# Performance work log

Measured on AMD Instinct MI355X. Metric: run time of the kernel, lower is better.

The kernel has to match this reference:

```python
import jax, jax.numpy as jnp
import numpy as np

INPUT, HIDDEN, OUTPUT = 128, 256, 128
BATCH, SEQ = 64, 2048


def setup_inputs() -> dict:
    key = jax.random.key(0)
    ks = jax.random.split(key, 7)
    s_ih = 1.0 / np.sqrt(HIDDEN)
    x = jax.random.normal(ks[0], (BATCH, SEQ, INPUT), dtype=jnp.float32)
    W_ih = jax.random.uniform(ks[1], (HIDDEN, INPUT), jnp.float32, -s_ih, s_ih)
    W_hh = jax.random.uniform(ks[2], (HIDDEN, HIDDEN), jnp.float32, -s_ih, s_ih)
    b_ih = jax.random.uniform(ks[3], (HIDDEN,), jnp.float32, -s_ih, s_ih)
    b_hh = jax.random.uniform(ks[4], (HIDDEN,), jnp.float32, -s_ih, s_ih)
    s_fc = 1.0 / np.sqrt(HIDDEN)
    W_fc = jax.random.uniform(ks[5], (OUTPUT, HIDDEN), jnp.float32, -s_fc, s_fc)
    b_fc = jax.random.uniform(ks[6], (OUTPUT,), jnp.float32, -s_fc, s_fc)
    return {"x": x, "W_ih": W_ih, "W_hh": W_hh, "b_ih": b_ih,
            "b_hh": b_hh, "W_fc": W_fc, "b_fc": b_fc}


def reference(x, W_ih, W_hh, b_ih, b_hh, W_fc, b_fc):
    B = x.shape[0]
    # Precompute input projections for all timesteps: [S, B, H]
    xp = jnp.einsum('bsi,hi->sbh', x, W_ih) + b_ih + b_hh
    h0 = jnp.zeros((B, W_hh.shape[0]), dtype=x.dtype)

    def step(h, xp_t):
        h = jnp.tanh(xp_t + h @ W_hh.T)
        return h, None

    hT, _ = jax.lax.scan(step, h0, xp)
    return hT @ W_fc.T + b_fc
```

## Files before the change

### kernel.cpp

```cpp
#include <hip/hip_runtime.h>
#include <hip/hip_bf16.h>
#include <hip/hip_fp16.h>


#define S_LEN 2048
#define B_SZ  64
#define IN_D  128
#define HID   256
#define OUT_D 128

typedef _Float16 half2_t __attribute__((ext_vector_type(2)));
typedef _Float16 half8_t __attribute__((ext_vector_type(8)));
typedef float    f32x4   __attribute__((ext_vector_type(4)));

#if __has_builtin(__builtin_amdgcn_fdot2)
#define FDOT2(a, b, c) __builtin_amdgcn_fdot2((a), (b), (c), false)
#else
#define FDOT2(a, b, c) ((c) + (float)(a).x * (float)(b).x + (float)(a).y * (float)(b).y)
#endif

#if __has_builtin(__builtin_amdgcn_exp2f)
#define EXP2F(x) __builtin_amdgcn_exp2f(x)
#else
#define EXP2F(x) exp2f(x)
#endif

#if __has_builtin(__builtin_amdgcn_rcpf)
#define RCPF(x) __builtin_amdgcn_rcpf(x)
#else
#define RCPF(x) (1.0f / (x))
#endif

__global__ __launch_bounds__(256) void xproj_kernel(
    const float* __restrict__ x, const float* __restrict__ W_ih,
    const float* __restrict__ b_ih, const float* __restrict__ b_hh,
    _Float16* __restrict__ xp)
{
    const int lane  = threadIdx.x & 63;
    const int wave  = threadIdx.x >> 6;
    const int idx16 = lane & 15;
    const int kq    = lane >> 4;
    const int r0    = blockIdx.x * 256 + wave * 64;

    half8_t afr[4][4];
    #pragma unroll
    for (int mt = 0; mt < 4; ++mt) {
        #pragma unroll
        for (int sl = 0; sl < 4; ++sl) {
            const float4* ap = (const float4*)(x + (size_t)(r0 + mt * 16 + idx16) * IN_D + sl * 32 + kq * 8);
            float4 a0 = ap[0], a1 = ap[1];
            afr[mt][sl] = half8_t{(_Float16)a0.x, (_Float16)a0.y, (_Float16)a0.z, (_Float16)a0.w,
                                  (_Float16)a1.x, (_Float16)a1.y, (_Float16)a1.z, (_Float16)a1.w};
        }
    }

    for (int nc = 0; nc < 16; ++nc) {
        const int n0 = nc * 16;
        const float bias = b_ih[n0 + idx16] + b_hh[n0 + idx16];

        half8_t bfr[4];
        #pragma unroll
        for (int sl = 0; sl < 4; ++sl) {
            const float4* bp = (const float4*)(W_ih + (size_t)(n0 + idx16) * IN_D + sl * 32 + kq * 8);
            float4 b0 = bp[0], b1 = bp[1];
            bfr[sl] = half8_t{(_Float16)b0.x, (_Float16)b0.y, (_Float16)b0.z, (_Float16)b0.w,
                              (_Float16)b1.x, (_Float16)b1.y, (_Float16)b1.z, (_Float16)b1.w};
        }

        #pragma unroll
        for (int mt = 0; mt < 4; ++mt) {
            f32x4 acc = {0.f, 0.f, 0.f, 0.f};
            #pragma unroll
            for (int sl = 0; sl < 4; ++sl)
                acc = __builtin_amdgcn_mfma_f32_16x16x32_f16(afr[mt][sl], bfr[sl], acc, 0, 0, 0);
            #pragma unroll
            for (int r = 0; r < 4; ++r) {
                const int m = r0 + mt * 16 + kq * 4 + r;
                xp[(size_t)m * HID + n0 + idx16] = (_Float16)(acc[r] + bias);
            }
        }
    }
}

__global__ __launch_bounds__(1024) void rnn_kernel(
    const _Float16* __restrict__ xp, const float* __restrict__ W_hh,
    const float* __restrict__ W_fc, const float* __restrict__ b_fc,
    float* __restrict__ out)
{
    const int b     = blockIdx.x;
    const int tid   = threadIdx.x;
    const int j     = tid & 255;
    const int slice = tid >> 8;

    __shared__ __align__(16) _Float16 hbuf[2][HID];
    __shared__ __align__(16) float    part[4][HID];

    half2_t w[32];
    {
        const float4* wr = (const float4*)(W_hh + (size_t)j * HID + slice * 64);
        #pragma unroll
        for (int c = 0; c < 16; ++c) {
            float4 v = wr[c];
            w[2 * c]     = half2_t{(_Float16)v.x, (_Float16)v.y};
            w[2 * c + 1] = half2_t{(_Float16)v.z, (_Float16)v.w};
        }
    }

    if (tid < HID) hbuf[0][tid] = (_Float16)0.f;

    const bool fin = (slice == (j >> 6));
    const _Float16* xpb = xp + (size_t)b * S_LEN * HID + j;
    float p0 = 0.f, p1 = 0.f;
    if (fin) { p0 = (float)xpb[0]; p1 = (float)xpb[HID]; }

    __syncthreads();

    for (int t = 0; t < S_LEN; ++t) {
        const int rb = t & 1;
        const float4* hp = (const float4*)&hbuf[rb][slice * 64];
        float a0 = 0.f, a1 = 0.f, a2 = 0.f, a3 = 0.f;
        #pragma unroll
        for (int c = 0; c < 8; ++c) {
            float4 hv = hp[c];
            union { float f; half2_t h; } u0, u1, u2, u3;
            u0.f = hv.x; u1.f = hv.y; u2.f = hv.z; u3.f = hv.w;
            a0 = FDOT2(w[4 * c + 0], u0.h, a0);
            a1 = FDOT2(w[4 * c + 1], u1.h, a1);
            a2 = FDOT2(w[4 * c + 2], u2.h, a2);
            a3 = FDOT2(w[4 * c + 3], u3.h, a3);
        }
        part[slice][j] = (a0 + a1) + (a2 + a3);
        __syncthreads();

        if (fin) {
            float z = part[0][j] + part[1][j] + part[2][j] + part[3][j] + p0;
            p0 = p1;
            const int tn = (t + 2 < S_LEN) ? (t + 2) : (S_LEN - 1);
            p1 = (float)xpb[(size_t)tn * HID];
            const float e = EXP2F(z * 2.8853900817779268f);
            hbuf[rb ^ 1][j] = (_Float16)(1.f - 2.f * RCPF(e + 1.f));
        }
        __syncthreads();
    }

    if (tid < OUT_D) {
        float acc2 = b_fc[tid];
        const float4* wp = (const float4*)(W_fc + (size_t)tid * HID);
        const _Float16* hf = hbuf[0];
        #pragma unroll 8
        for (int c = 0; c < 64; ++c) {
            float4 wv = wp[c];
            acc2 += wv.x * (float)hf[4 * c + 0] + wv.y * (float)hf[4 * c + 1] +
                    wv.z * (float)hf[4 * c + 2] + wv.w * (float)hf[4 * c + 3];
        }
        out[(size_t)b * OUT_D + tid] = acc2;
    }
}

extern "C" void kernel_launch(void* const* d_in, const int* in_sizes, int n_in,
                              void* d_out, int out_size, void* d_ws, size_t ws_size,
                              hipStream_t stream) {
    const float* x    = (const float*)d_in[0];
    const float* W_ih = (const float*)d_in[1];
    const float* W_hh = (const float*)d_in[2];
    const float* b_ih = (const float*)d_in[3];
    const float* b_hh = (const float*)d_in[4];
    const float* W_fc = (const float*)d_in[5];
    const float* b_fc = (const float*)d_in[6];
    float* outp = (float*)d_out;

    _Float16* xp_ws = (_Float16*)d_ws;

    dim3 gA(S_LEN * B_SZ / 256, 1, 1);
    xproj_kernel<<<gA, 256, 0, stream>>>(x, W_ih, b_ih, b_hh, xp_ws);

    rnn_kernel<<<B_SZ, 1024, 0, stream>>>(xp_ws, W_hh, W_fc, b_fc, outp);
}
```

Before: 1.553 ms.

## Batch 16 sequences per block and compute recurrence with MFMA

The recurrent kernel now processes 16 batch rows per block, 4 blocks total, and computes h@W_hh^T with 16x16x32 f16 MFMA instructions using W_hh held in registers. This replaces 64 blocks of per-sequence fdot2 dot products and the shared-memory partial-sum reduction with its extra barrier. Each step now needs one barrier instead of two. The FC head also moves to MFMA. The trade-off is far fewer blocks on the GPU (4 instead of 64), so the serial per-step latency of the MFMA chain plus the tanh and store work sets the runtime, and occupancy across CUs is very low.

```diff
diff --git a/kernel.cpp b/kernel.cpp
--- a/kernel.cpp
+++ b/kernel.cpp
@@ -8,16 +8,10 @@
 #define IN_D  128
 #define HID   256
 #define OUT_D 128
-
-typedef _Float16 half2_t __attribute__((ext_vector_type(2)));
+#define HPAD  264
+
 typedef _Float16 half8_t __attribute__((ext_vector_type(8)));
 typedef float    f32x4   __attribute__((ext_vector_type(4)));
-
-#if __has_builtin(__builtin_amdgcn_fdot2)
-#define FDOT2(a, b, c) __builtin_amdgcn_fdot2((a), (b), (c), false)
-#else
-#define FDOT2(a, b, c) ((c) + (float)(a).x * (float)(b).x + (float)(a).y * (float)(b).y)
-#endif
 
 #if __has_builtin(__builtin_amdgcn_exp2f)
 #define EXP2F(x) __builtin_amdgcn_exp2f(x)
@@ -82,78 +76,138 @@
     }
 }
 
-__global__ __launch_bounds__(1024) void rnn_kernel(
+template <int CUR>
+static __device__ __forceinline__ void rnn_step(
+    _Float16 (*hl)[16][HPAD],
+    const half8_t (&B)[4][8],
+    _Float16 (&pc)[16],
+    const _Float16* const (&xb)[4],
+    int t, int c16, int g, int wave)
+{
+    half8_t A[8];
+    #pragma unroll
+    for (int s = 0; s < 8; ++s)
+        A[s] = *(const half8_t*)&hl[CUR][c16][32 * s + g * 8];
+
+    f32x4 C0 = {0.f,0.f,0.f,0.f}, C1 = {0.f,0.f,0.f,0.f};
+    f32x4 C2 = {0.f,0.f,0.f,0.f}, C3 = {0.f,0.f,0.f,0.f};
+    #pragma unroll
+    for (int s = 0; s < 8; ++s) {
+        C0 = __builtin_amdgcn_mfma_f32_16x16x32_f16(A[s], B[0][s], C0, 0, 0, 0);
+        C1 = __builtin_amdgcn_mfma_f32_16x16x32_f16(A[s], B[1][s], C1, 0, 0, 0);
+        C2 = __builtin_amdgcn_mfma_f32_16x16x32_f16(A[s], B[2][s], C2, 0, 0, 0);
+        C3 = __builtin_amdgcn_mfma_f32_16x16x32_f16(A[s], B[3][s], C3, 0, 0, 0);
+    }
+
+    #pragma unroll
+    for (int nt = 0; nt < 4; ++nt) {
+        f32x4 Cv = (nt == 0) ? C0 : (nt == 1) ? C1 : (nt == 2) ? C2 : C3;
+        #pragma unroll
+        for (int r = 0; r < 4; ++r) {
+            const float z = Cv[r] + (float)pc[r * 4 + nt];
+            const float e = EXP2F(z * 2.8853900817779268f);
+            const float th = 1.f - 2.f * RCPF(e + 1.f);
+            hl[CUR ^ 1][g * 4 + r][wave * 64 + nt * 16 + c16] = (_Float16)th;
+        }
+    }
+
+    if (t + 2 < S_LEN) {
+        #pragma unroll
+        for (int r = 0; r < 4; ++r)
+            #pragma unroll
+            for (int nt = 0; nt < 4; ++nt)
+                pc[r * 4 + nt] = xb[r][(size_t)(t + 2) * HID + nt * 16];
+    }
+
+    __syncthreads();
+}
+
+__global__ __launch_bounds__(256)
+__attribute__((amdgpu_waves_per_eu(1, 1)))
+void rnn_kernel(
     const _Float16* __restrict__ xp, const float* __restrict__ W_hh,
     const float* __restrict__ W_fc, const float* __restrict__ b_fc,
     float* __restrict__ out)
 {
-    const int b     = blockIdx.x;
-    const int tid   = threadIdx.x;
-    const int j     = tid & 255;
-    const int slice = tid >> 8;
-
-    __shared__ __align__(16) _Float16 hbuf[2][HID];
-    __shared__ __align__(16) float    part[4][HID];
-
-    half2_t w[32];
-    {
-        const float4* wr = (const float4*)(W_hh + (size_t)j * HID + slice * 64);
-        #pragma unroll
-        for (int c = 0; c < 16; ++c) {
-            float4 v = wr[c];
-            w[2 * c]     = half2_t{(_Float16)v.x, (_Float16)v.y};
-            w[2 * c + 1] = half2_t{(_Float16)v.z, (_Float16)v.w};
-        }
-    }
-
-    if (tid < HID) hbuf[0][tid] = (_Float16)0.f;
-
-    const bool fin = (slice == (j >> 6));
-    const _Float16* xpb = xp + (size_t)b * S_LEN * HID + j;
-    float p0 = 0.f, p1 = 0.f;
-    if (fin) { p0 = (float)xpb[0]; p1 = (float)xpb[HID]; }
+    const int tid  = threadIdx.x;
+    const int lane = tid & 63;
+    const int wave = tid >> 6;
+    const int m0   = blockIdx.x * 16;
+    const int c16  = lane & 15;
+    const int g    = lane >> 4;
+
+    __shared__ __align__(16) _Float16 hlds[2][16][HPAD];
+
+    half8_t B[4][8];
+    #pragma unroll
+    for (int nt = 0; nt < 4; ++nt) {
+        const float* wrow = W_hh + (size_t)(wave * 64 + nt * 16 + c16) * HID + g * 8;
+        #pragma unroll
+        for (int s = 0; s < 8; ++s) {
+            const float4* p = (const float4*)(wrow + 32 * s);
+            float4 v0 = p[0], v1 = p[1];
+            B[nt][s] = half8_t{(_Float16)v0.x, (_Float16)v0.y, (_Float16)v0.z, (_Float16)v0.w,
+                               (_Float16)v1.x, (_Float16)v1.y, (_Float16)v1.z, (_Float16)v1.w};
+        }
+    }
+
+    for (int i = tid; i < 16 * HPAD; i += 256)
+        ((_Float16*)hlds)[i] = (_Float16)0.f;
+
+    const _Float16* xb[4];
+    #pragma unroll
+    for (int r = 0; r < 4; ++r)
+        xb[r] = xp + (size_t)(m0 + g * 4 + r) * S_LEN * HID + wave * 64 + c16;
+
+    _Float16 pA[16], pB[16];
+    #pragma unroll
+    for (int r = 0; r < 4; ++r) {
+        #pragma unroll
+        for (int nt = 0; nt < 4; ++nt) {
+            pA[r * 4 + nt] = xb[r][nt * 16];
+            pB[r * 4 + nt] = xb[r][(size_t)HID + nt * 16];
+        }
+    }
 
     __syncthreads();
 
-    for (int t = 0; t < S_LEN; ++t) {
-        const int rb = t & 1;
-        const float4* hp = (const float4*)&hbuf[rb][slice * 64];
-        float a0 = 0.f, a1 = 0.f, a2 = 0.f, a3 = 0.f;
-        #pragma unroll
-        for (int c = 0; c < 8; ++c) {
-            float4 hv = hp[c];
-            union { float f; half2_t h; } u0, u1, u2, u3;
-            u0.f = hv.x; u1.f = hv.y; u2.f = hv.z; u3.f = hv.w;
-            a0 = FDOT2(w[4 * c + 0], u0.h, a0);
-            a1 = FDOT2(w[4 * c + 1], u1.h, a1);
-            a2 = FDOT2(w[4 * c + 2], u2.h, a2);
-            a3 = FDOT2(w[4 * c + 3], u3.h, a3);
-        }
-        part[slice][j] = (a0 + a1) + (a2 + a3);
-        __syncthreads();
-
-        if (fin) {
-            float z = part[0][j] + part[1][j] + part[2][j] + part[3][j] + p0;
-            p0 = p1;
-            const int tn = (t + 2 < S_LEN) ? (t + 2) : (S_LEN - 1);
-            p1 = (float)xpb[(size_t)tn * HID];
-            const float e = EXP2F(z * 2.8853900817779268f);
-            hbuf[rb ^ 1][j] = (_Float16)(1.f - 2.f * RCPF(e + 1.f));
-        }
-        __syncthreads();
-    }
-
-    if (tid < OUT_D) {
-        float acc2 = b_fc[tid];
-        const float4* wp = (const float4*)(W_fc + (size_t)tid * HID);
-        const _Float16* hf = hbuf[0];
-        #pragma unroll 8
-        for (int c = 0; c < 64; ++c) {
-            float4 wv = wp[c];
-            acc2 += wv.x * (float)hf[4 * c + 0] + wv.y * (float)hf[4 * c + 1] +
-                    wv.z * (float)hf[4 * c + 2] + wv.w * (float)hf[4 * c + 3];
-        }
-        out[(size_t)b * OUT_D + tid] = acc2;
+    for (int t = 0; t < S_LEN; t += 2) {
+        rnn_step<0>(hlds, B, pA, xb, t,     c16, g, wave);
+        rnn_step<1>(hlds, B, pB, xb, t + 1, c16, g, wave);
+    }
+
+    half8_t Bf[2][8];
+    #pragma unroll
+    for (int nt = 0; nt < 2; ++nt) {
+        const float* wrow = W_fc + (size_t)(wave * 32 + nt * 16 + c16) * HID + g * 8;
+        #pragma unroll
+        for (int s = 0; s < 8; ++s) {
+            const float4* p = (const float4*)(wrow + 32 * s);
+            float4 v0 = p[0], v1 = p[1];
+            Bf[nt][s] = half8_t{(_Float16)v0.x, (_Float16)v0.y, (_Float16)v0.z, (_Float16)v0.w,
+                                (_Float16)v1.x, (_Float16)v1.y, (_Float16)v1.z, (_Float16)v1.w};
+        }
+    }
+    half8_t A[8];
+    #pragma unroll
+    for (int s = 0; s < 8; ++s)
+        A[s] = *(const half8_t*)&hlds[0][c16][32 * s + g * 8];
+
+    f32x4 D0 = {0.f,0.f,0.f,0.f}, D1 = {0.f,0.f,0.f,0.f};
+    #pragma unroll
+    for (int s = 0; s < 8; ++s) {
+        D0 = __builtin_amdgcn_mfma_f32_16x16x32_f16(A[s], Bf[0][s], D0, 0, 0, 0);
+        D1 = __builtin_amdgcn_mfma_f32_16x16x32_f16(A[s], Bf[1][s], D1, 0, 0, 0);
+    }
+    #pragma unroll
+    for (int nt = 0; nt < 2; ++nt) {
+        f32x4 Dv = (nt == 0) ? D0 : D1;
+        const int o = wave * 32 + nt * 16 + c16;
+        #pragma unroll
+        for (int r = 0; r < 4; ++r) {
+            const int b = m0 + g * 4 + r;
+            out[(size_t)b * OUT_D + o] = Dv[r] + b_fc[o];
+        }
     }
 }
 
@@ -174,5 +228,5 @@
     dim3 gA(S_LEN * B_SZ / 256, 1, 1);
     xproj_kernel<<<gA, 256, 0, stream>>>(x, W_ih, b_ih, b_hh, xp_ws);
 
-    rnn_kernel<<<B_SZ, 1024, 0, stream>>>(xp_ws, W_hh, W_fc, b_fc, outp);
-}
+    rnn_kernel<<<4, 256, 0, stream>>>(xp_ws, W_hh, W_fc, b_fc, outp);
+}
```

Result: slower. 2.407 ms (+55.0%).
